# Kernel tuning notes

Measured on AMD Instinct MI355X. Metric: run time of the kernel, lower is better.

## Reference

```python
import jax, jax.numpy as jnp
import numpy as np

B, G, D, V = 4, 2048, 256, 60000


def setup_inputs() -> dict:
    key = jax.random.key(0)
    k1, k2, k3, k4, k5 = jax.random.split(key, 5)
    gene_ids = jax.random.randint(k1, (B, G), 0, V, dtype=jnp.int64 if jax.config.jax_enable_x64 else jnp.int32)
    emb_table = jax.random.normal(k2, (V, D), dtype=jnp.float32) * 0.02
    w_proj = jax.random.normal(k3, (2 * D,), dtype=jnp.float32) * (1.0 / np.sqrt(2 * D))
    b_proj = jnp.zeros((), dtype=jnp.float32)
    gate_logits = jax.random.normal(k4, (G * G,), dtype=jnp.float32)
    class_logits = jax.random.normal(k5, (G * G, 3), dtype=jnp.float32)
    return {"gene_ids": gene_ids, "emb_table": emb_table, "w_proj": w_proj,
            "b_proj": b_proj, "gate_logits": gate_logits, "class_logits": class_logits}


def reference(gene_ids, emb_table, w_proj, b_proj, gate_logits, class_logits):
    # Gene embedding lookup: (B, G, D)
    e = emb_table[gene_ids]
    d = e.shape[-1]
    # Linear(2d,1) on cat([e_i, e_j]) == <e_i, w[:d]> + <e_j, w[d:]> + b,
    # broadcast-added over the (i, j) grid — no (B,G,G,2D) concat needed.
    s_i = jnp.einsum("bgd,d->bg", e, w_proj[:d])  # (B, G)
    s_j = jnp.einsum("bgd,d->bg", e, w_proj[d:])  # (B, G)
    interaction = s_i[:, :, None] + s_j[:, None, :] + b_proj  # (B, G, G)

    g = interaction.shape[1]
    # L0 gate, eval mode: hard threshold of sigmoid(gate_logits)
    gate_probs = (jax.nn.sigmoid(gate_logits) > 0.5).astype(e.dtype)  # (G*G,)
    sparse = interaction * gate_probs.reshape(1, g, g)

    # Three-way classifier, eval mode: hard one-hot of argmax(softmax(logits))
    class_probs = jax.nn.one_hot(jnp.argmax(class_logits, axis=-1), 3, dtype=e.dtype)  # (G*G, 3)
    class_values = class_probs @ jnp.array([-1.0, 0.0, 1.0], dtype=e.dtype)  # (G*G,)
    regulatory = sparse * class_values.reshape(1, g, g)

    l0_reg = jnp.sum(jax.nn.sigmoid(gate_logits))
    return (e, interaction, sparse, regulatory, gate_probs, class_probs, l0_reg)
```

## Files before the change

### kernel.cpp

```cpp
#include <hip/hip_runtime.h>

#define BB 4
#define GN 2048
#define DD 256
#define GG (GN * GN)

#define OFF_E   0u
#define OFF_INT 2097152u
#define OFF_SP  18874368u
#define OFF_RG  35651584u
#define OFF_GP  52428800u
#define OFF_CP  56623104u
#define OFF_L0  69206016u

__global__ __launch_bounds__(64) void k_embed(
    const int* __restrict__ gene_ids, const float* __restrict__ emb,
    const float* __restrict__ w, float* __restrict__ e_out,
    float* __restrict__ s_i, float* __restrict__ s_j) {
  const int row  = blockIdx.x;
  const int lane = threadIdx.x;
  const int gid  = gene_ids[row];

  const float4 v  = ((const float4*)(emb + (size_t)gid * DD))[lane];
  ((float4*)(e_out + (size_t)row * DD))[lane] = v;

  const float4 w0 = ((const float4*)w)[lane];
  const float4 w1 = ((const float4*)(w + DD))[lane];
  float di = v.x * w0.x + v.y * w0.y + v.z * w0.z + v.w * w0.w;
  float dj = v.x * w1.x + v.y * w1.y + v.z * w1.z + v.w * w1.w;
#pragma unroll
  for (int off = 32; off > 0; off >>= 1) {
    di += __shfl_down(di, off);
    dj += __shfl_down(dj, off);
  }
  if (lane == 0) { s_i[row] = di; s_j[row] = dj; }
}

__device__ __forceinline__ int argmax3(float a, float b, float c) {
  int idx = 0; float best = a;
  if (b > best) { best = b; idx = 1; }
  if (c > best) { idx = 2; }
  return idx;
}
__device__ __forceinline__ float sigf(float x) { return 1.0f / (1.0f + __expf(-x)); }

__global__ __launch_bounds__(256) void k_gate(
    const float* __restrict__ gl, const float* __restrict__ cl,
    float* __restrict__ gate_out, float* __restrict__ cp_out,
    unsigned char* __restrict__ code, float* __restrict__ l0) {
  const int t = blockIdx.x * 256 + threadIdx.x;
  const float4 g = ((const float4*)gl)[t];
  const float4* clp = (const float4*)cl + (size_t)t * 3;
  const float4 c0 = clp[0], c1 = clp[1], c2 = clp[2];

  const int i0 = argmax3(c0.x, c0.y, c0.z);
  const int i1 = argmax3(c0.w, c1.x, c1.y);
  const int i2 = argmax3(c1.z, c1.w, c2.x);
  const int i3 = argmax3(c2.y, c2.z, c2.w);

  const float gx = g.x > 0.0f ? 1.0f : 0.0f;
  const float gy = g.y > 0.0f ? 1.0f : 0.0f;
  const float gz = g.z > 0.0f ? 1.0f : 0.0f;
  const float gw = g.w > 0.0f ? 1.0f : 0.0f;

  ((float4*)gate_out)[t] = make_float4(gx, gy, gz, gw);

  float4* cpo = (float4*)cp_out + (size_t)t * 3;
  cpo[0] = make_float4(i0 == 0, i0 == 1, i0 == 2, i1 == 0);
  cpo[1] = make_float4(i1 == 1, i1 == 2, i2 == 0, i2 == 1);
  cpo[2] = make_float4(i2 == 2, i3 == 0, i3 == 1, i3 == 2);

  ((uchar4*)code)[t] = make_uchar4(
      (unsigned char)((int)gx | (i0 << 4)), (unsigned char)((int)gy | (i1 << 4)),
      (unsigned char)((int)gz | (i2 << 4)), (unsigned char)((int)gw | (i3 << 4)));

  float s = sigf(g.x) + sigf(g.y) + sigf(g.z) + sigf(g.w);
#pragma unroll
  for (int off = 32; off > 0; off >>= 1) s += __shfl_down(s, off);
  __shared__ float part[4];
  if ((threadIdx.x & 63) == 0) part[threadIdx.x >> 6] = s;
  __syncthreads();
  if (threadIdx.x == 0) atomicAdd(l0, part[0] + part[1] + part[2] + part[3]);
}

__global__ __launch_bounds__(256) void k_bcast(
    const float* __restrict__ s_i, const float* __restrict__ s_j,
    const float* __restrict__ bptr, const unsigned char* __restrict__ code,
    float* __restrict__ inter, float* __restrict__ sparse,
    float* __restrict__ reg) {
  const int t  = blockIdx.x * 256 + threadIdx.x;
  const int j4 = t & (GN / 4 - 1);
  const int i  = (t >> 9) & (GN - 1);
  const int b  = t >> 20;

  const float  si = s_i[b * GN + i] + bptr[0];
  const float4 sj = ((const float4*)(s_j + b * GN))[j4];
  const uchar4 cd = ((const uchar4*)(code + (size_t)i * GN))[j4];

  const float4 it4 = make_float4(si + sj.x, si + sj.y, si + sj.z, si + sj.w);
  const float4 sp4 = make_float4(it4.x * (float)(cd.x & 15), it4.y * (float)(cd.y & 15),
                                 it4.z * (float)(cd.z & 15), it4.w * (float)(cd.w & 15));
  const float4 rg4 = make_float4(sp4.x * (float)((cd.x >> 4) - 1), sp4.y * (float)((cd.y >> 4) - 1),
                                 sp4.z * (float)((cd.z >> 4) - 1), sp4.w * (float)((cd.w >> 4) - 1));

  ((float4*)inter)[t]  = it4;
  ((float4*)sparse)[t] = sp4;
  ((float4*)reg)[t]    = rg4;
}

extern "C" void kernel_launch(void* const* d_in, const int* in_sizes, int n_in,
                              void* d_out, int out_size, void* d_ws, size_t ws_size,
                              hipStream_t stream) {
  const int*   gene_ids = (const int*)d_in[0];
  const float* emb      = (const float*)d_in[1];
  const float* w        = (const float*)d_in[2];
  const float* bptr     = (const float*)d_in[3];
  const float* gl       = (const float*)d_in[4];
  const float* cl       = (const float*)d_in[5];
  float* out = (float*)d_out;

  float* s_i = (float*)d_ws;
  float* s_j = s_i + BB * GN;
  unsigned char* code = (unsigned char*)d_ws + 65536;

  hipMemsetAsync(out + OFF_L0, 0, sizeof(float), stream);

  k_embed<<<BB * GN, 64, 0, stream>>>(gene_ids, emb, w, out + OFF_E, s_i, s_j);
  k_gate<<<GG / 1024, 256, 0, stream>>>(gl, cl, out + OFF_GP, out + OFF_CP,
                                        code, out + OFF_L0);
  k_bcast<<<(BB * GG / 4) / 256, 256, 0, stream>>>(s_i, s_j, bptr, code,
                                                   out + OFF_INT, out + OFF_SP,
                                                   out + OFF_RG);
}
```

Measured before the change: 392.6 us.

## Fuse gate and broadcast kernels, add nontemporal loads/stores

Merges the gate/classifier kernel with the broadcast kernel, so each thread computes the gate and class codes and then writes interaction, sparse and regulatory for all four batches directly. This removes the intermediate byte-code buffer round trip and one kernel launch. It also uses nontemporal loads and stores for streaming data and packs four embedding rows per 256-thread block. Each thread now does more stores, which reduces parallelism per element.

```diff
diff --git a/kernel.cpp b/kernel.cpp
--- a/kernel.cpp
+++ b/kernel.cpp
@@ -13,16 +13,27 @@
 #define OFF_CP  56623104u
 #define OFF_L0  69206016u
 
-__global__ __launch_bounds__(64) void k_embed(
+typedef float nat4 __attribute__((ext_vector_type(4)));
+
+__device__ __forceinline__ void nt_store4(float* p, float4 v) {
+  nat4 n = {v.x, v.y, v.z, v.w};
+  __builtin_nontemporal_store(n, (nat4*)p);
+}
+__device__ __forceinline__ float4 nt_load4(const float* p) {
+  nat4 n = __builtin_nontemporal_load((const nat4*)p);
+  return make_float4(n.x, n.y, n.z, n.w);
+}
+
+__global__ __launch_bounds__(256) void k_embed(
     const int* __restrict__ gene_ids, const float* __restrict__ emb,
     const float* __restrict__ w, float* __restrict__ e_out,
     float* __restrict__ s_i, float* __restrict__ s_j) {
-  const int row  = blockIdx.x;
-  const int lane = threadIdx.x;
+  const int row  = blockIdx.x * 4 + (threadIdx.x >> 6);
+  const int lane = threadIdx.x & 63;
   const int gid  = gene_ids[row];
 
-  const float4 v  = ((const float4*)(emb + (size_t)gid * DD))[lane];
-  ((float4*)(e_out + (size_t)row * DD))[lane] = v;
+  const float4 v = ((const float4*)(emb + (size_t)gid * DD))[lane];
+  nt_store4(e_out + (size_t)row * DD + lane * 4, v);
 
   const float4 w0 = ((const float4*)w)[lane];
   const float4 w1 = ((const float4*)(w + DD))[lane];
@@ -44,14 +55,21 @@
 }
 __device__ __forceinline__ float sigf(float x) { return 1.0f / (1.0f + __expf(-x)); }
 
-__global__ __launch_bounds__(256) void k_gate(
+__global__ __launch_bounds__(256) void k_fused(
     const float* __restrict__ gl, const float* __restrict__ cl,
+    const float* __restrict__ s_i, const float* __restrict__ s_j,
+    const float* __restrict__ bptr,
     float* __restrict__ gate_out, float* __restrict__ cp_out,
-    unsigned char* __restrict__ code, float* __restrict__ l0) {
-  const int t = blockIdx.x * 256 + threadIdx.x;
-  const float4 g = ((const float4*)gl)[t];
-  const float4* clp = (const float4*)cl + (size_t)t * 3;
-  const float4 c0 = clp[0], c1 = clp[1], c2 = clp[2];
+    float* __restrict__ inter, float* __restrict__ sparse,
+    float* __restrict__ reg, float* __restrict__ l0) {
+  const int t  = blockIdx.x * 256 + threadIdx.x;
+  const int j4 = t & (GN / 4 - 1);
+  const int i  = t >> 9;
+
+  const float4 g  = nt_load4(gl + (size_t)t * 4);
+  const float4 c0 = nt_load4(cl + (size_t)t * 12);
+  const float4 c1 = nt_load4(cl + (size_t)t * 12 + 4);
+  const float4 c2 = nt_load4(cl + (size_t)t * 12 + 8);
 
   const int i0 = argmax3(c0.x, c0.y, c0.z);
   const int i1 = argmax3(c0.w, c1.x, c1.y);
@@ -63,16 +81,30 @@
   const float gz = g.z > 0.0f ? 1.0f : 0.0f;
   const float gw = g.w > 0.0f ? 1.0f : 0.0f;
 
-  ((float4*)gate_out)[t] = make_float4(gx, gy, gz, gw);
+  nt_store4(gate_out + (size_t)t * 4, make_float4(gx, gy, gz, gw));
+  nt_store4(cp_out + (size_t)t * 12,
+            make_float4(i0 == 0, i0 == 1, i0 == 2, i1 == 0));
+  nt_store4(cp_out + (size_t)t * 12 + 4,
+            make_float4(i1 == 1, i1 == 2, i2 == 0, i2 == 1));
+  nt_store4(cp_out + (size_t)t * 12 + 8,
+            make_float4(i2 == 2, i3 == 0, i3 == 1, i3 == 2));
 
-  float4* cpo = (float4*)cp_out + (size_t)t * 3;
-  cpo[0] = make_float4(i0 == 0, i0 == 1, i0 == 2, i1 == 0);
-  cpo[1] = make_float4(i1 == 1, i1 == 2, i2 == 0, i2 == 1);
-  cpo[2] = make_float4(i2 == 2, i3 == 0, i3 == 1, i3 == 2);
+  const float vx = (float)(i0 - 1), vy = (float)(i1 - 1);
+  const float vz = (float)(i2 - 1), vw = (float)(i3 - 1);
+  const float b0 = bptr[0];
 
-  ((uchar4*)code)[t] = make_uchar4(
-      (unsigned char)((int)gx | (i0 << 4)), (unsigned char)((int)gy | (i1 << 4)),
-      (unsigned char)((int)gz | (i2 << 4)), (unsigned char)((int)gw | (i3 << 4)));
+#pragma unroll
+  for (int b = 0; b < BB; ++b) {
+    const float  si = s_i[b * GN + i] + b0;
+    const float4 sj = ((const float4*)(s_j + b * GN))[j4];
+    const float4 it4 = make_float4(si + sj.x, si + sj.y, si + sj.z, si + sj.w);
+    const float4 sp4 = make_float4(it4.x * gx, it4.y * gy, it4.z * gz, it4.w * gw);
+    const float4 rg4 = make_float4(sp4.x * vx, sp4.y * vy, sp4.z * vz, sp4.w * vw);
+    const size_t o = (size_t)b * (GG / 4) + t;
+    nt_store4(inter  + o * 4, it4);
+    nt_store4(sparse + o * 4, sp4);
+    nt_store4(reg    + o * 4, rg4);
+  }
 
   float s = sigf(g.x) + sigf(g.y) + sigf(g.z) + sigf(g.w);
 #pragma unroll
@@ -81,31 +113,6 @@
   if ((threadIdx.x & 63) == 0) part[threadIdx.x >> 6] = s;
   __syncthreads();
   if (threadIdx.x == 0) atomicAdd(l0, part[0] + part[1] + part[2] + part[3]);
-}
-
-__global__ __launch_bounds__(256) void k_bcast(
-    const float* __restrict__ s_i, const float* __restrict__ s_j,
-    const float* __restrict__ bptr, const unsigned char* __restrict__ code,
-    float* __restrict__ inter, float* __restrict__ sparse,
-    float* __restrict__ reg) {
-  const int t  = blockIdx.x * 256 + threadIdx.x;
-  const int j4 = t & (GN / 4 - 1);
-  const int i  = (t >> 9) & (GN - 1);
-  const int b  = t >> 20;
-
-  const float  si = s_i[b * GN + i] + bptr[0];
-  const float4 sj = ((const float4*)(s_j + b * GN))[j4];
-  const uchar4 cd = ((const uchar4*)(code + (size_t)i * GN))[j4];
-
-  const float4 it4 = make_float4(si + sj.x, si + sj.y, si + sj.z, si + sj.w);
-  const float4 sp4 = make_float4(it4.x * (float)(cd.x & 15), it4.y * (float)(cd.y & 15),
-                                 it4.z * (float)(cd.z & 15), it4.w * (float)(cd.w & 15));
-  const float4 rg4 = make_float4(sp4.x * (float)((cd.x >> 4) - 1), sp4.y * (float)((cd.y >> 4) - 1),
-                                 sp4.z * (float)((cd.z >> 4) - 1), sp4.w * (float)((cd.w >> 4) - 1));
-
-  ((float4*)inter)[t]  = it4;
-  ((float4*)sparse)[t] = sp4;
-  ((float4*)reg)[t]    = rg4;
 }
 
 extern "C" void kernel_launch(void* const* d_in, const int* in_sizes, int n_in,
@@ -121,14 +128,12 @@
 
   float* s_i = (float*)d_ws;
   float* s_j = s_i + BB * GN;
-  unsigned char* code = (unsigned char*)d_ws + 65536;
 
-  hipMemsetAsync(out + OFF_L0, 0, sizeof(float), stream);
+  (void)hipMemsetAsync(out + OFF_L0, 0, sizeof(float), stream);
 
-  k_embed<<<BB * GN, 64, 0, stream>>>(gene_ids, emb, w, out + OFF_E, s_i, s_j);
-  k_gate<<<GG / 1024, 256, 0, stream>>>(gl, cl, out + OFF_GP, out + OFF_CP,
-                                        code, out + OFF_L0);
-  k_bcast<<<(BB * GG / 4) / 256, 256, 0, stream>>>(s_i, s_j, bptr, code,
-                                                   out + OFF_INT, out + OFF_SP,
-                                                   out + OFF_RG);
+  k_embed<<<BB * GN / 4, 256, 0, stream>>>(gene_ids, emb, w, out + OFF_E, s_i, s_j);
+  k_fused<<<GG / 1024, 256, 0, stream>>>(gl, cl, s_i, s_j, bptr,
+                                         out + OFF_GP, out + OFF_CP,
+                                         out + OFF_INT, out + OFF_SP,
+                                         out + OFF_RG, out + OFF_L0);
 }
```

Result: no change. 397.3 us (+1.2%).
